# Kernel tuning notes

Measured on AMD Instinct MI355X. Metric: run time of the kernel, lower is better.

The kernel has to match this reference:

```python
import jax, jax.numpy as jnp
import numpy as np
from jax import lax

H = 1024   # hidden_size
T = 512    # input_len
P = 96     # pred_len
B = 256    # batch


def _lstm_cell(x, h, c, Wih, Whh, b):
    # PyTorch gate order: i, f, g, o
    gates = x @ Wih.T + h @ Whh.T + b          # [B, 4H]
    i, f, g, o = jnp.split(gates, 4, axis=-1)
    i, f, o = jax.nn.sigmoid(i), jax.nn.sigmoid(f), jax.nn.sigmoid(o)
    g = jnp.tanh(g)
    c = f * c + i * g
    h = o * jnp.tanh(c)
    return h, c


def setup_inputs() -> dict:
    key = jax.random.key(0)
    ks = jax.random.split(key, 10)
    s = 1.0 / np.sqrt(H)
    u = lambda k, shape: jax.random.uniform(k, shape, jnp.float32, -s, s)
    return {
        "input_seq": jax.random.normal(ks[0], (B, T, 1), jnp.float32),
        # encoder LSTM params (b = b_ih + b_hh, identical math)
        "enc_Wih": u(ks[1], (4 * H, 1)),
        "enc_Whh": u(ks[2], (4 * H, H)),
        "enc_b":   u(ks[3], (4 * H,)),
        # learned initial states (nn.Parameter zeros)
        "h0": jnp.zeros((H,), jnp.float32),
        "c0": jnp.zeros((H,), jnp.float32),
        # decoder LSTMCell params
        "dec_Wih": u(ks[4], (4 * H, 1)),
        "dec_Whh": u(ks[5], (4 * H, H)),
        "dec_b":   u(ks[6], (4 * H,)),
        # decoder output projection Linear(H, 1)
        "out_W": u(ks[7], (1, H)),
        "out_b": u(ks[8], (1,)),
    }


def reference(input_seq, enc_Wih, enc_Whh, enc_b, h0, c0,
              dec_Wih, dec_Whh, dec_b, out_W, out_b):
    bsz = input_seq.shape[0]
    h = jnp.broadcast_to(h0, (bsz, H))
    c = jnp.broadcast_to(c0, (bsz, H))

    # ---- encoder: single-layer LSTM over T steps ----
    def enc_step(carry, x_t):           # x_t: [B, 1]
        h, c = carry
        h, c = _lstm_cell(x_t, h, c, enc_Wih, enc_Whh, enc_b)
        return (h, c), None
    (h, c), _ = lax.scan(enc_step, (h, c), jnp.transpose(input_seq, (1, 0, 2)))

    dec_in = input_seq[:, -1, :]        # [B, 1]

    def dec_step(carry, _):
        dec_in, h, c = carry
        h, c = _lstm_cell(dec_in, h, c, dec_Wih, dec_Whh, dec_b)
        out = h @ out_W.T + out_b       # [B, 1]
        return (out, h, c), out[:, 0]
    _, ys = lax.scan(dec_step, (dec_in, h, c), None, length=P)  # ys: [P, B]

    return ys.T[:, :, None]             # [B, P, 1]
```

## Files before the change

kernel.cpp:

```cpp
#include <hip/hip_runtime.h>

constexpr int kH = 1024;
constexpr int kT = 512;
constexpr int kP = 96;
constexpr int kB = 256;
constexpr int kSteps = kT + kP;
constexpr unsigned NB = 256;

__device__ __forceinline__ float sig_(float x) { return 1.0f / (1.0f + __expf(-x)); }
__device__ __forceinline__ float tanh_(float x) {
  float e = __expf(-2.0f * fabsf(x));
  float t = (1.0f - e) / (1.0f + e);
  return copysignf(t, x);
}

__device__ __forceinline__ float gload(const float* p) {
  return __hip_atomic_load(const_cast<float*>(p), __ATOMIC_RELAXED,
                           __HIP_MEMORY_SCOPE_AGENT);
}
__device__ __forceinline__ void gstore(float* p, float v) {
  __hip_atomic_store(p, v, __ATOMIC_RELAXED, __HIP_MEMORY_SCOPE_AGENT);
}

__device__ __forceinline__ void gbar(unsigned* cnt, unsigned target) {
  __syncthreads();
  if (threadIdx.x == 0) {
    __hip_atomic_fetch_add(cnt, 1u, __ATOMIC_RELAXED, __HIP_MEMORY_SCOPE_AGENT);
    while (__hip_atomic_load(cnt, __ATOMIC_RELAXED, __HIP_MEMORY_SCOPE_AGENT) < target)
      __builtin_amdgcn_s_sleep(2);
  }
  __syncthreads();
}

__global__ void zero_cnt(unsigned* cnt) { if (threadIdx.x == 0) *cnt = 0u; }

__global__ void __launch_bounds__(1024, 4)
lstm4(const float* __restrict__ xin,
      const float* __restrict__ eWih,
      const float* __restrict__ eWhh,
      const float* __restrict__ eb,
      const float* __restrict__ h0,
      const float* __restrict__ c0,
      const float* __restrict__ dWih,
      const float* __restrict__ dWhh,
      const float* __restrict__ db,
      const float* __restrict__ outW,
      const float* __restrict__ outb,
      float* __restrict__ out,
      float* __restrict__ hA,
      float* __restrict__ hB,
      float* __restrict__ xT,
      float* __restrict__ gpart,
      float* __restrict__ decout,
      unsigned* __restrict__ cnt)
{
  const int tid  = threadIdx.x;
  const int bid  = blockIdx.x;
  const int j0   = bid * 4;
  const int lane = tid & 63;
  const int wvu  = __builtin_amdgcn_readfirstlane(tid >> 6);
  const int ks   = wvu & 7;
  const int rg   = wvu >> 3;
  const int jj   = tid >> 8;
  const int bb   = tid & 255;

  __shared__ float part[8][16][256];
  __shared__ float decl[4][256];
  __shared__ float redw[4];

  gstore(&hA[(j0 + jj) * kB + bb], h0[j0 + jj]);
  float cReg    = c0[j0 + jj];
  float outWreg = outW[j0 + jj];
  const float outb0 = outb[0];
  {
    int g = bid * 1024 + tid;
    if (g < kT * kB) gstore(&xT[g], xin[(g & 255) * kT + (g >> 8)]);
  }

  int rowbase[8];
#pragma unroll
  for (int rr = 0; rr < 8; ++rr) {
    int r = rg * 8 + rr;
    rowbase[rr] = ((r >> 2) * kH + j0 + (r & 3)) * kH;
  }

  const float* __restrict__ Whh  = eWhh;
  const float* __restrict__ Wih  = eWih;
  const float* __restrict__ bias = eb;
  float* hc = hA;
  float* hn = hB;

  unsigned bt = NB;
  gbar(cnt, bt); bt += NB;

  for (int step = 0; step < kSteps; ++step) {
    const bool dec = (step >= kT);
    if (step == kT) { Whh = dWhh; Wih = dWih; bias = db; }

    if (dec && step > kT) {
      float p = 0.0f;
      if (tid < kB) p = gload(&gpart[bid * kB + tid]);
#pragma unroll
      for (int off = 32; off > 0; off >>= 1) p += __shfl_down(p, off, 64);
      if (tid < kB && (tid & 63) == 0) redw[tid >> 6] = p;
      __syncthreads();
      if (tid == 0) {
        float y = ((redw[0] + redw[1]) + redw[2]) + redw[3] + outb0;
        out[bid * kP + (step - 1 - kT)] = y;
        gstore(&decout[bid], y);
      }
    }

    float acc[8][4];
#pragma unroll
    for (int rr = 0; rr < 8; ++rr)
#pragma unroll
      for (int q = 0; q < 4; ++q) acc[rr][q] = 0.f;

    const int k0 = ks * 128;
    for (int kk = 0; kk < 128; kk += 2) {
      const int k = k0 + kk;
      float2 w2[8];
#pragma unroll
      for (int rr = 0; rr < 8; ++rr)
        w2[rr] = *(const float2*)&Whh[rowbase[rr] + k];
      float h2[2][4];
#pragma unroll
      for (int dk = 0; dk < 2; ++dk)
#pragma unroll
        for (int q = 0; q < 4; ++q)
          h2[dk][q] = gload(&hc[(k + dk) * kB + q * 64 + lane]);
#pragma unroll
      for (int rr = 0; rr < 8; ++rr)
#pragma unroll
        for (int q = 0; q < 4; ++q) {
          acc[rr][q] = fmaf(w2[rr].x, h2[0][q], acc[rr][q]);
          acc[rr][q] = fmaf(w2[rr].y, h2[1][q], acc[rr][q]);
        }
    }

#pragma unroll
    for (int rr = 0; rr < 8; ++rr)
#pragma unroll
      for (int q = 0; q < 4; ++q)
        part[ks][rg * 8 + rr][q * 64 + lane] = acc[rr][q];

    if (dec) { gbar(cnt, bt); bt += NB; }
    else     { __syncthreads(); }

    float xv;
    if (!dec)            xv = gload(&xT[step * kB + bb]);
    else if (step == kT) xv = gload(&xT[(kT - 1) * kB + bb]);
    else                 xv = gload(&decout[bb]);

    float g4[4];
#pragma unroll
    for (int g = 0; g < 4; ++g) {
      const int r = g * 4 + jj;
      float s = part[0][r][bb];
#pragma unroll
      for (int k2 = 1; k2 < 8; ++k2) s += part[k2][r][bb];
      const int grow = g * kH + j0 + jj;
      g4[g] = s + bias[grow] + xv * Wih[grow];
    }
    float ig = sig_(g4[0]), fg = sig_(g4[1]);
    float gg = tanh_(g4[2]), og = sig_(g4[3]);
    cReg = fg * cReg + ig * gg;
    float hv = og * tanh_(cReg);
    gstore(&hn[(j0 + jj) * kB + bb], hv);

    if (dec) {
      decl[jj][bb] = hv * outWreg;
      __syncthreads();
      if (tid < kB) {
        float s = ((decl[0][tid] + decl[1][tid]) + decl[2][tid]) + decl[3][tid];
        gstore(&gpart[tid * kB + bid], s);
      }
    }

    gbar(cnt, bt); bt += NB;
    float* tmp = hc; hc = hn; hn = tmp;
  }

  {
    float p = 0.0f;
    if (tid < kB) p = gload(&gpart[bid * kB + tid]);
#pragma unroll
    for (int off = 32; off > 0; off >>= 1) p += __shfl_down(p, off, 64);
    if (tid < kB && (tid & 63) == 0) redw[tid >> 6] = p;
    __syncthreads();
    if (tid == 0)
      out[bid * kP + (kP - 1)] = ((redw[0] + redw[1]) + redw[2]) + redw[3] + outb0;
  }
}

extern "C" void kernel_launch(void* const* d_in, const int* in_sizes, int n_in,
                              void* d_out, int out_size, void* d_ws, size_t ws_size,
                              hipStream_t stream) {
  const float* xin  = (const float*)d_in[0];
  const float* eWih = (const float*)d_in[1];
  const float* eWhh = (const float*)d_in[2];
  const float* eb   = (const float*)d_in[3];
  const float* h0   = (const float*)d_in[4];
  const float* c0   = (const float*)d_in[5];
  const float* dWih = (const float*)d_in[6];
  const float* dWhh = (const float*)d_in[7];
  const float* db   = (const float*)d_in[8];
  const float* outW = (const float*)d_in[9];
  const float* outb = (const float*)d_in[10];
  float* out = (float*)d_out;

  float* wsf    = (float*)d_ws;
  float* hA     = wsf;
  float* hB     = hA + kH * kB;
  float* xT     = hB + kH * kB;
  float* gpart  = xT + kT * kB;
  float* decout = gpart + kB * 256;
  unsigned* cnt = (unsigned*)(decout + kB);

  zero_cnt<<<1, 64, 0, stream>>>(cnt);

  void* args[] = {(void*)&xin, (void*)&eWih, (void*)&eWhh, (void*)&eb,
                  (void*)&h0, (void*)&c0, (void*)&dWih, (void*)&dWhh,
                  (void*)&db, (void*)&outW, (void*)&outb, (void*)&out,
                  (void*)&hA, (void*)&hB, (void*)&xT, (void*)&gpart,
                  (void*)&decout, (void*)&cnt};
  hipLaunchCooperativeKernel((const void*)lstm4, dim3(256), dim3(1024),
                             args, 0, stream);
}
```

Baseline: 27.42 ms.

## Retile LSTM recurrence into 16-unit by 64-batch blocks with double-buffered decoder output

Each block now owns 16 hidden units across a 64-sample batch tile instead of 4 units across all 256 samples. Each wave covers a 64-wide K slice with 64 accumulators per thread, and K partials are combined in shared memory in four serialized phases. The decoder projection partials are double-buffered in global memory, so the extra grid barrier each decoder step is removed and the feedback value is read locally. The change cuts h reloads per weight but raises register pressure (64 accumulators under launch bounds of 1024 threads) and may cause spills, and weights are re-read by four batch-tile blocks.

```diff
diff --git a/kernel.cpp b/kernel.cpp
--- a/kernel.cpp
+++ b/kernel.cpp
@@ -5,6 +5,8 @@
 constexpr int kP = 96;
 constexpr int kB = 256;
 constexpr int kSteps = kT + kP;
+constexpr int UN = 16;
+constexpr int BT = 64;
 constexpr unsigned NB = 256;
 
 __device__ __forceinline__ float sig_(float x) { return 1.0f / (1.0f + __expf(-x)); }
@@ -35,7 +37,7 @@
 __global__ void zero_cnt(unsigned* cnt) { if (threadIdx.x == 0) *cnt = 0u; }
 
 __global__ void __launch_bounds__(1024, 4)
-lstm4(const float* __restrict__ xin,
+lstm5(const float* __restrict__ xin,
       const float* __restrict__ eWih,
       const float* __restrict__ eWhh,
       const float* __restrict__ eb,
@@ -51,37 +53,28 @@
       float* __restrict__ hB,
       float* __restrict__ xT,
       float* __restrict__ gpart,
-      float* __restrict__ decout,
       unsigned* __restrict__ cnt)
 {
   const int tid  = threadIdx.x;
   const int bid  = blockIdx.x;
-  const int j0   = bid * 4;
+  const int rg   = (bid & 7) * 8 + (bid >> 5);
+  const int tile = (bid >> 3) & 3;
+  const int j0   = rg * UN;
+  const int b0   = tile * BT;
   const int lane = tid & 63;
-  const int wvu  = __builtin_amdgcn_readfirstlane(tid >> 6);
-  const int ks   = wvu & 7;
-  const int rg   = wvu >> 3;
-  const int jj   = tid >> 8;
-  const int bb   = tid & 255;
-
-  __shared__ float part[8][16][256];
-  __shared__ float decl[4][256];
-  __shared__ float redw[4];
-
-  gstore(&hA[(j0 + jj) * kB + bb], h0[j0 + jj]);
-  float cReg    = c0[j0 + jj];
-  float outWreg = outW[j0 + jj];
+  const int wv   = __builtin_amdgcn_readfirstlane(tid >> 6);
+
+  __shared__ float part[4][64][64];
+  __shared__ float decl[16][64];
+  __shared__ float ybuf[64];
+
+  gstore(&hA[(j0 + wv) * kB + b0 + lane], h0[j0 + wv]);
+  float cReg    = c0[j0 + wv];
+  float outWreg = outW[j0 + wv];
   const float outb0 = outb[0];
   {
     int g = bid * 1024 + tid;
     if (g < kT * kB) gstore(&xT[g], xin[(g & 255) * kT + (g >> 8)]);
-  }
-
-  int rowbase[8];
-#pragma unroll
-  for (int rr = 0; rr < 8; ++rr) {
-    int r = rg * 8 + rr;
-    rowbase[rr] = ((r >> 2) * kH + j0 + (r & 3)) * kH;
   }
 
   const float* __restrict__ Whh  = eWhh;
@@ -98,99 +91,123 @@
     if (step == kT) { Whh = dWhh; Wih = dWih; bias = db; }
 
     if (dec && step > kT) {
-      float p = 0.0f;
-      if (tid < kB) p = gload(&gpart[bid * kB + tid]);
-#pragma unroll
-      for (int off = 32; off > 0; off >>= 1) p += __shfl_down(p, off, 64);
-      if (tid < kB && (tid & 63) == 0) redw[tid >> 6] = p;
+      const int rp = (step - 1 - kT) & 1;
+      const float* gp = gpart + (rp * 4 + tile) * 64 * 64;
+      float p4 = 0.f;
+#pragma unroll
+      for (int i = 0; i < 4; ++i)
+        p4 += gload(&gp[(wv * 4 + i) * 64 + lane]);
+      decl[wv][lane] = p4;
       __syncthreads();
-      if (tid == 0) {
-        float y = ((redw[0] + redw[1]) + redw[2]) + redw[3] + outb0;
-        out[bid * kP + (step - 1 - kT)] = y;
-        gstore(&decout[bid], y);
+      if (tid < 64) {
+        float y = outb0;
+#pragma unroll
+        for (int c2 = 0; c2 < 16; ++c2) y += decl[c2][tid];
+        ybuf[tid] = y;
+        if (rg == 0) out[(b0 + tid) * kP + (step - 1 - kT)] = y;
       }
     }
 
-    float acc[8][4];
-#pragma unroll
-    for (int rr = 0; rr < 8; ++rr)
-#pragma unroll
-      for (int q = 0; q < 4; ++q) acc[rr][q] = 0.f;
-
-    const int k0 = ks * 128;
-    for (int kk = 0; kk < 128; kk += 2) {
+    float acc[64];
+#pragma unroll
+    for (int r = 0; r < 64; ++r) acc[r] = 0.f;
+
+    const int k0 = wv * 64;
+    for (int kk = 0; kk < 64; kk += 8) {
       const int k = k0 + kk;
-      float2 w2[8];
-#pragma unroll
-      for (int rr = 0; rr < 8; ++rr)
-        w2[rr] = *(const float2*)&Whh[rowbase[rr] + k];
-      float h2[2][4];
-#pragma unroll
-      for (int dk = 0; dk < 2; ++dk)
-#pragma unroll
-        for (int q = 0; q < 4; ++q)
-          h2[dk][q] = gload(&hc[(k + dk) * kB + q * 64 + lane]);
-#pragma unroll
-      for (int rr = 0; rr < 8; ++rr)
-#pragma unroll
-        for (int q = 0; q < 4; ++q) {
-          acc[rr][q] = fmaf(w2[rr].x, h2[0][q], acc[rr][q]);
-          acc[rr][q] = fmaf(w2[rr].y, h2[1][q], acc[rr][q]);
-        }
-    }
-
-#pragma unroll
-    for (int rr = 0; rr < 8; ++rr)
-#pragma unroll
-      for (int q = 0; q < 4; ++q)
-        part[ks][rg * 8 + rr][q * 64 + lane] = acc[rr][q];
-
-    if (dec) { gbar(cnt, bt); bt += NB; }
-    else     { __syncthreads(); }
+      float h8[8];
+#pragma unroll
+      for (int d = 0; d < 8; ++d)
+        h8[d] = gload(&hc[(k + d) * kB + b0 + lane]);
+#pragma unroll
+      for (int r = 0; r < 64; ++r) {
+        const float* wp = &Whh[((r >> 4) * kH + j0 + (r & 15)) * kH + k];
+        float4 wa = *(const float4*)wp;
+        float4 wb = *(const float4*)(wp + 4);
+        acc[r] = fmaf(wa.x, h8[0], acc[r]);
+        acc[r] = fmaf(wa.y, h8[1], acc[r]);
+        acc[r] = fmaf(wa.z, h8[2], acc[r]);
+        acc[r] = fmaf(wa.w, h8[3], acc[r]);
+        acc[r] = fmaf(wb.x, h8[4], acc[r]);
+        acc[r] = fmaf(wb.y, h8[5], acc[r]);
+        acc[r] = fmaf(wb.z, h8[6], acc[r]);
+        acc[r] = fmaf(wb.w, h8[7], acc[r]);
+      }
+    }
+
+    const int slot = wv & 3, ph = wv >> 2;
+    if (ph == 0) {
+#pragma unroll
+      for (int r = 0; r < 64; ++r) part[slot][r][lane] = acc[r];
+    }
+    __syncthreads();
+    if (ph == 1) {
+#pragma unroll
+      for (int r = 0; r < 64; ++r) part[slot][r][lane] += acc[r];
+    }
+    __syncthreads();
+    if (ph == 2) {
+#pragma unroll
+      for (int r = 0; r < 64; ++r) part[slot][r][lane] += acc[r];
+    }
+    __syncthreads();
+    if (ph == 3) {
+#pragma unroll
+      for (int r = 0; r < 64; ++r) part[slot][r][lane] += acc[r];
+    }
+    __syncthreads();
 
     float xv;
-    if (!dec)            xv = gload(&xT[step * kB + bb]);
-    else if (step == kT) xv = gload(&xT[(kT - 1) * kB + bb]);
-    else                 xv = gload(&decout[bb]);
+    if (!dec)            xv = gload(&xT[step * kB + b0 + lane]);
+    else if (step == kT) xv = gload(&xT[(kT - 1) * kB + b0 + lane]);
+    else                 xv = ybuf[lane];
 
     float g4[4];
 #pragma unroll
     for (int g = 0; g < 4; ++g) {
-      const int r = g * 4 + jj;
-      float s = part[0][r][bb];
-#pragma unroll
-      for (int k2 = 1; k2 < 8; ++k2) s += part[k2][r][bb];
-      const int grow = g * kH + j0 + jj;
+      const int r = g * UN + wv;
+      float s = ((part[0][r][lane] + part[1][r][lane]) +
+                 part[2][r][lane]) + part[3][r][lane];
+      const int grow = g * kH + j0 + wv;
       g4[g] = s + bias[grow] + xv * Wih[grow];
     }
     float ig = sig_(g4[0]), fg = sig_(g4[1]);
     float gg = tanh_(g4[2]), og = sig_(g4[3]);
     cReg = fg * cReg + ig * gg;
     float hv = og * tanh_(cReg);
-    gstore(&hn[(j0 + jj) * kB + bb], hv);
+    gstore(&hn[(j0 + wv) * kB + b0 + lane], hv);
 
     if (dec) {
-      decl[jj][bb] = hv * outWreg;
+      decl[wv][lane] = hv * outWreg;
       __syncthreads();
-      if (tid < kB) {
-        float s = ((decl[0][tid] + decl[1][tid]) + decl[2][tid]) + decl[3][tid];
-        gstore(&gpart[tid * kB + bid], s);
+      if (tid < 64) {
+        float p = 0.f;
+#pragma unroll
+        for (int u = 0; u < 16; ++u) p += decl[u][tid];
+        const int wp2 = (step - kT) & 1;
+        gstore(&gpart[((wp2 * 4 + tile) * 64 + rg) * 64 + tid], p);
       }
     }
 
     gbar(cnt, bt); bt += NB;
-    float* tmp = hc; hc = hn; hn = tmp;
-  }
-
-  {
-    float p = 0.0f;
-    if (tid < kB) p = gload(&gpart[bid * kB + tid]);
-#pragma unroll
-    for (int off = 32; off > 0; off >>= 1) p += __shfl_down(p, off, 64);
-    if (tid < kB && (tid & 63) == 0) redw[tid >> 6] = p;
-    __syncthreads();
-    if (tid == 0)
-      out[bid * kP + (kP - 1)] = ((redw[0] + redw[1]) + redw[2]) + redw[3] + outb0;
+    float* t2 = hc; hc = hn; hn = t2;
+  }
+
+  if (rg == 0) {
+    const int rp = (kP - 1) & 1;
+    const float* gp = gpart + (rp * 4 + tile) * 64 * 64;
+    float p4 = 0.f;
+#pragma unroll
+    for (int i = 0; i < 4; ++i)
+      p4 += gload(&gp[(wv * 4 + i) * 64 + lane]);
+    decl[wv][lane] = p4;
+    __syncthreads();
+    if (tid < 64) {
+      float y = outb0;
+#pragma unroll
+      for (int c2 = 0; c2 < 16; ++c2) y += decl[c2][tid];
+      out[(b0 + tid) * kP + (kP - 1)] = y;
+    }
   }
 }
 
@@ -215,8 +232,7 @@
   float* hB     = hA + kH * kB;
   float* xT     = hB + kH * kB;
   float* gpart  = xT + kT * kB;
-  float* decout = gpart + kB * 256;
-  unsigned* cnt = (unsigned*)(decout + kB);
+  unsigned* cnt = (unsigned*)(gpart + 2 * 4 * 64 * 64);
 
   zero_cnt<<<1, 64, 0, stream>>>(cnt);
 
@@ -224,7 +240,7 @@
                   (void*)&h0, (void*)&c0, (void*)&dWih, (void*)&dWhh,
                   (void*)&db, (void*)&outW, (void*)&outb, (void*)&out,
                   (void*)&hA, (void*)&hB, (void*)&xT, (void*)&gpart,
-                  (void*)&decout, (void*)&cnt};
-  hipLaunchCooperativeKernel((const void*)lstm4, dim3(256), dim3(1024),
+                  (void*)&cnt};
+  hipLaunchCooperativeKernel((const void*)lstm5, dim3(256), dim3(1024),
                              args, 0, stream);
 }
```

Result: slower. 43.04 ms (+57.0%).
